# Performance work log

Measured on AMD Instinct MI355X. Metric: run time of the kernel, lower is better.

The kernel has to match this reference:

```python
import jax, jax.numpy as jnp
import numpy as np

B, T, F, H = 4096, 48, 64, 128


def _uniform(key, shape, stdv):
    return jax.random.uniform(key, shape, jnp.float32, -stdv, stdv)


def setup_inputs() -> dict:
    key = jax.random.key(0)
    ks = jax.random.split(key, 24)
    values = jax.random.normal(ks[0], (B, T, F), jnp.float32)
    masks = (jax.random.uniform(ks[1], (B, T, F)) < 0.8).astype(jnp.float32)
    deltas = jax.random.uniform(ks[2], (B, T, F), jnp.float32)
    sH = 1.0 / np.sqrt(H)
    sF = 1.0 / np.sqrt(F)
    inp = {
        "values": values, "masks": masks, "deltas": deltas,
        # TemporalDecay h: W [H, F], b [H] (stdv = 1/sqrt(out=H))
        "Wdh": _uniform(ks[3], (H, F), sH), "bdh": _uniform(ks[4], (H,), sH),
        # TemporalDecay x (diag): W [F, F], b [F]
        "Wdx": _uniform(ks[5], (F, F), sF), "bdx": _uniform(ks[6], (F,), sF),
        # hist_reg: Linear(H -> F)
        "Wh": _uniform(ks[7], (F, H), sH), "bh": _uniform(ks[8], (F,), sH),
        # feat_reg: masked F x F
        "Wf": _uniform(ks[9], (F, F), sF), "bf": _uniform(ks[10], (F,), sF),
        # weight_combine: Linear(2F -> F)
        "Wc": _uniform(ks[11], (F, 2 * F), 1.0 / np.sqrt(2 * F)),
        "bc": _uniform(ks[12], (F,), 1.0 / np.sqrt(2 * F)),
        # LSTMCell(2F -> H): gates in PyTorch order i, f, g, o
        "W_ih": _uniform(ks[13], (4 * H, 2 * F), sH),
        "W_hh": _uniform(ks[14], (4 * H, H), sH),
        "b_ih": _uniform(ks[15], (4 * H,), sH),
        "b_hh": _uniform(ks[16], (4 * H,), sH),
        # out: Linear(H -> 1)
        "Wo": _uniform(ks[17], (1, H), sH), "bo": _uniform(ks[18], (1,), sH),
    }
    return inp


def reference(values, masks, deltas, Wdh, bdh, Wdx, bdx, Wh, bh, Wf, bf,
              Wc, bc, W_ih, W_hh, b_ih, b_hh, Wo, bo):
    impute_weight = 1.0
    b, t, f = values.shape
    h_dim = Wdh.shape[0]
    eye = jnp.eye(f, dtype=values.dtype)
    Wdx_m = Wdx * eye            # diagonal temporal decay
    Wf_m = Wf * (1.0 - eye)

    def step(carry, xt):
        h, c, loss = carry
        x, m, d = xt  # each [B, F]
        gamma_h = jnp.exp(-jax.nn.relu(d @ Wdh.T + bdh))        # [B, H]
        gamma_x = jnp.exp(-jax.nn.relu(d @ Wdx_m.T + bdx))      # [B, F]
        h = h * gamma_h
        x_h = h @ Wh.T + bh
        denom = jnp.sum(m) + 1e-5
        loss = loss + jnp.sum(jnp.abs(x - x_h) * m) / denom
        x_c = m * x + (1.0 - m) * x_h
        z_h = x_c @ Wf_m.T + bf
        loss = loss + jnp.sum(jnp.abs(x - z_h) * m) / denom
        alpha = jnp.concatenate([gamma_x, m], axis=1) @ Wc.T + bc
        c_h = alpha * z_h + (1.0 - alpha) * x_h
        loss = loss + jnp.sum(jnp.abs(x - c_h) * m) / denom
        c_c = m * x + (1.0 - m) * c_h
        inputs = jnp.concatenate([c_c, m], axis=1)  # [B, 2F]
        gates = inputs @ W_ih.T + b_ih + h @ W_hh.T + b_hh
        i_g, f_g, g_g, o_g = jnp.split(gates, 4, axis=1)
        c = jax.nn.sigmoid(f_g) * c + jax.nn.sigmoid(i_g) * jnp.tanh(g_g)
        h = jax.nn.sigmoid(o_g) * jnp.tanh(c)
        return (h, c, loss), c_c

    init = (jnp.zeros((b, h_dim), values.dtype),
            jnp.zeros((b, h_dim), values.dtype),
            jnp.zeros((), values.dtype))
    xs = (jnp.swapaxes(values, 0, 1),
          jnp.swapaxes(masks, 0, 1),
          jnp.swapaxes(deltas, 0, 1))
    (h, c, x_loss), imps = jax.lax.scan(step, init, xs)
    imputations = jnp.swapaxes(imps, 0, 1)  # [B, T, F]
    predictions = h @ Wo.T + bo             # [B, 1]
    return x_loss * impute_weight, imputations, predictions
```

## Files before the change

### kernel.cpp

```cpp
#include <hip/hip_runtime.h>
#include <hip/hip_bf16.h>
#include <math.h>

#define BB 4096
#define TT 48
#define FF 64
#define HH 128
#define ROWS 16
#define NT 512
#define NBLK (BB / ROWS)

typedef __attribute__((ext_vector_type(8))) short short8;
typedef __attribute__((ext_vector_type(4))) float f32x4;

__device__ __forceinline__ float sigm(float x) { return 1.f / (1.f + __expf(-x)); }
__device__ __forceinline__ float tanh_f(float x) { return 2.f / (1.f + __expf(-2.f * x)) - 1.f; }

__global__ __launch_bounds__(256) void prep_kernel(
    const float* __restrict__ W_ih, const float* __restrict__ W_hh,
    const float* __restrict__ Wdh,  const float* __restrict__ Wh,
    const float* __restrict__ Wf,   const float* __restrict__ Wc,
    __hip_bfloat16* __restrict__ frags) {
    const int idx = blockIdx.x * 256 + threadIdx.x;
    float v;
    if (idx < 131072) {
        const int jj = idx & 7;
        const int lane = (idx >> 3) & 63;
        const int ks = (idx >> 9) & 7;
        const int tile = idx >> 12;
        const int n = tile * 16 + (lane & 15);
        const int k = ks * 32 + ((lane >> 4) << 3) + jj;
        v = (k < 128) ? W_ih[n * 128 + k] : W_hh[n * 128 + (k - 128)];
    } else {
        const int u = idx - 131072;
        const int jj = u & 7;
        const int lane = (u >> 3) & 63;
        const int lq = lane & 15, q8 = (lane >> 4) << 3;
        if (u < 8192) {
            const int ks = (u >> 9) & 1, nt = u >> 10;
            const int n = nt * 16 + lq, k = ks * 32 + q8 + jj;
            v = Wdh[n * 64 + k];
        } else if (u < 16384) {
            const int uu = u - 8192;
            const int ks = (uu >> 9) & 3, nt = uu >> 11;
            const int n = nt * 16 + lq, k = ks * 32 + q8 + jj;
            v = Wh[n * 128 + k];
        } else if (u < 20480) {
            const int uu = u - 16384;
            const int ks = (uu >> 9) & 1, nt = uu >> 10;
            const int n = nt * 16 + lq, k = ks * 32 + q8 + jj;
            v = (k == n) ? 0.f : Wf[n * 64 + k];
        } else {
            const int uu = u - 20480;
            const int ks = (uu >> 9) & 3, nt = uu >> 11;
            const int n = nt * 16 + lq, k = ks * 32 + q8 + jj;
            v = Wc[n * 128 + k];
        }
    }
    frags[idx] = __float2bfloat16(v);
}

__global__ __launch_bounds__(NT, 2) void rits_kernel(
    const float* __restrict__ values, const float* __restrict__ masks,
    const float* __restrict__ deltas,
    const float* __restrict__ Wdx, const float* __restrict__ bdx,
    const float* __restrict__ bdh, const float* __restrict__ bh,
    const float* __restrict__ bf,  const float* __restrict__ bc,
    const float* __restrict__ b_ih, const float* __restrict__ b_hh,
    const float* __restrict__ Wo,  const float* __restrict__ bo,
    const __hip_bfloat16* __restrict__ frags,
    float* __restrict__ ws_msum,
    float* __restrict__ ws_numer,
    float* __restrict__ out_imp, float* __restrict__ out_pred)
{
    __shared__ __hip_bfloat16 dbuf[ROWS][72];
    __shared__ __hip_bfloat16 xcbuf[ROWS][72];
    __shared__ __hip_bfloat16 hbuf[ROWS][136];
    __shared__ __hip_bfloat16 gxm[ROWS][136];
    __shared__ __hip_bfloat16 ccm[ROWS][136];
    __shared__ float x_lds[ROWS][65];
    __shared__ float m_lds[ROWS][65];
    __shared__ float redm[8];
    __shared__ float redl[8];

    const int tid = threadIdx.x;
    const int bid = blockIdx.x;
    const int b0 = bid * ROWS;
    const int lane = tid & 63;
    const int wv = tid >> 6;
    const int quad = lane >> 4;
    const int lq = lane & 15;

    for (int i = tid; i < ROWS * 136; i += NT) ((unsigned short*)hbuf)[i] = 0;

    const float wdx_l = Wdx[lane * (FF + 1)];
    const float bdx_l = bdx[lane];

    const int j_ln = wv * 16 + lq;
    const float bdh_j = bdh[j_ln];
    const float bI = b_ih[j_ln]       + b_hh[j_ln];
    const float bF = b_ih[128 + j_ln] + b_hh[128 + j_ln];
    const float bG = b_ih[256 + j_ln] + b_hh[256 + j_ln];
    const float bO = b_ih[384 + j_ln] + b_hh[384 + j_ln];

    const int f46 = (wv & 3) * 16 + lq;
    const float bh_f = bh[f46];
    const float bf_f = bf[f46];
    const float bc_f = bc[f46];

    const short8* f8 = (const short8*)frags;

    float c_reg[4];
    #pragma unroll
    for (int r = 0; r < 4; ++r) c_reg[r] = 0.f;

    __syncthreads();

    for (int t = 0; t < TT; ++t) {
        float msum_th = 0.f;
        #pragma unroll
        for (int q = 0; q < 2; ++q) {
            const int r = wv + 8 * q;
            const int off = ((b0 + r) * TT + t) * FF + lane;
            const float xv = values[off], mv = masks[off], dv = deltas[off];
            x_lds[r][lane] = xv;
            m_lds[r][lane] = mv;
            msum_th += mv;
            dbuf[r][lane] = __float2bfloat16(dv);
            const float gx = __expf(-fmaxf(fmaf(dv, wdx_l, bdx_l), 0.f));
            gxm[r][lane] = __float2bfloat16(gx);
            const __hip_bfloat16 mb = __float2bfloat16(mv);
            gxm[r][64 + lane] = mb;
            ccm[r][64 + lane] = mb;
        }
        #pragma unroll
        for (int off = 32; off; off >>= 1) msum_th += __shfl_down(msum_th, off, 64);
        if (lane == 0) redm[wv] = msum_th;
        __syncthreads();
        if (tid == 0) {
            float s = 0.f;
            #pragma unroll
            for (int w = 0; w < 8; ++w) s += redm[w];
            ws_msum[t * NBLK + bid] = s;
        }

        {
            f32x4 acc = {0.f, 0.f, 0.f, 0.f};
            #pragma unroll
            for (int ks = 0; ks < 2; ++ks) {
                const short8 a = *(const short8*)&dbuf[lq][ks * 32 + quad * 8];
                const short8 b = f8[16384 + ((wv * 2 + ks) << 6) + lane];
                acc = __builtin_amdgcn_mfma_f32_16x16x32_bf16(a, b, acc, 0, 0, 0);
            }
            #pragma unroll
            for (int r = 0; r < 4; ++r) {
                const int row = quad * 4 + r;
                const float gh = __expf(-fmaxf(acc[r] + bdh_j, 0.f));
                const float hd = __bfloat162float(hbuf[row][j_ln]) * gh;
                hbuf[row][j_ln] = __float2bfloat16(hd);
            }
        }
        __syncthreads();

        float xv_r[4], mv_r[4], xh_r[4];
        float stepsum = 0.f;

        if (wv < 4) {
            f32x4 acc = {0.f, 0.f, 0.f, 0.f};
            #pragma unroll
            for (int ks = 0; ks < 4; ++ks) {
                const short8 a = *(const short8*)&hbuf[lq][ks * 32 + quad * 8];
                const short8 b = f8[17408 + ((wv * 4 + ks) << 6) + lane];
                acc = __builtin_amdgcn_mfma_f32_16x16x32_bf16(a, b, acc, 0, 0, 0);
            }
            #pragma unroll
            for (int r = 0; r < 4; ++r) {
                const int row = quad * 4 + r;
                const float xh = acc[r] + bh_f;
                xh_r[r] = xh;
                const float xv = x_lds[row][f46], mv = m_lds[row][f46];
                xv_r[r] = xv; mv_r[r] = mv;
                stepsum += mv * fabsf(xv - xh);
                xcbuf[row][f46] = __float2bfloat16(fmaf(mv, xv, (1.f - mv) * xh));
            }
        }
        __syncthreads();

        if (wv < 4) {
            f32x4 acc5 = {0.f, 0.f, 0.f, 0.f};
            #pragma unroll
            for (int ks = 0; ks < 2; ++ks) {
                const short8 a = *(const short8*)&xcbuf[lq][ks * 32 + quad * 8];
                const short8 b = f8[18432 + ((wv * 2 + ks) << 6) + lane];
                acc5 = __builtin_amdgcn_mfma_f32_16x16x32_bf16(a, b, acc5, 0, 0, 0);
            }
            f32x4 acc6 = {0.f, 0.f, 0.f, 0.f};
            #pragma unroll
            for (int ks = 0; ks < 4; ++ks) {
                const short8 a = *(const short8*)&gxm[lq][ks * 32 + quad * 8];
                const short8 b = f8[18944 + ((wv * 4 + ks) << 6) + lane];
                acc6 = __builtin_amdgcn_mfma_f32_16x16x32_bf16(a, b, acc6, 0, 0, 0);
            }
            #pragma unroll
            for (int r = 0; r < 4; ++r) {
                const int row = quad * 4 + r;
                const float zh = acc5[r] + bf_f;
                stepsum += mv_r[r] * fabsf(xv_r[r] - zh);
                const float alpha = acc6[r] + bc_f;
                const float ch = fmaf(alpha, zh, (1.f - alpha) * xh_r[r]);
                stepsum += mv_r[r] * fabsf(xv_r[r] - ch);
                const float cc = fmaf(mv_r[r], xv_r[r], (1.f - mv_r[r]) * ch);
                ccm[row][f46] = __float2bfloat16(cc);
                out_imp[((b0 + row) * TT + t) * FF + f46] = cc;
            }
        }
        #pragma unroll
        for (int off = 32; off; off >>= 1) stepsum += __shfl_down(stepsum, off, 64);
        if (lane == 0) redl[wv] = stepsum;
        __syncthreads();
        if (tid == 0) {
            float s = 0.f;
            #pragma unroll
            for (int w = 0; w < 8; ++w) s += redl[w];
            ws_numer[t * NBLK + bid] = s;
        }

        {
            f32x4 acc[4];
            #pragma unroll
            for (int g = 0; g < 4; ++g) acc[g] = (f32x4){0.f, 0.f, 0.f, 0.f};
            #pragma unroll
            for (int ks = 0; ks < 8; ++ks) {
                const short8 a = (ks < 4)
                    ? *(const short8*)&ccm[lq][ks * 32 + quad * 8]
                    : *(const short8*)&hbuf[lq][(ks - 4) * 32 + quad * 8];
                #pragma unroll
                for (int g = 0; g < 4; ++g) {
                    const short8 b = f8[(((g * 8 + wv) * 8 + ks) << 6) + lane];
                    acc[g] = __builtin_amdgcn_mfma_f32_16x16x32_bf16(a, b, acc[g], 0, 0, 0);
                }
            }
            float hnew[4];
            #pragma unroll
            for (int r = 0; r < 4; ++r) {
                const float ig = sigm(acc[0][r] + bI);
                const float fg = sigm(acc[1][r] + bF);
                const float gg = tanh_f(acc[2][r] + bG);
                const float og = sigm(acc[3][r] + bO);
                c_reg[r] = fmaf(fg, c_reg[r], ig * gg);
                hnew[r] = og * tanh_f(c_reg[r]);
            }
            __syncthreads();
            #pragma unroll
            for (int r = 0; r < 4; ++r)
                hbuf[quad * 4 + r][j_ln] = __float2bfloat16(hnew[r]);
        }
        __syncthreads();
    }

    {
        const int r = tid >> 5, l = tid & 31;
        float s = 0.f;
        #pragma unroll
        for (int k = l; k < HH; k += 32) s += __bfloat162float(hbuf[r][k]) * Wo[k];
        #pragma unroll
        for (int off = 16; off; off >>= 1) s += __shfl_down(s, off, 32);
        if (l == 0) out_pred[b0 + r] = s + bo[0];
    }
}

__global__ __launch_bounds__(256) void final_kernel(const float* __restrict__ ws_msum,
                                                    const float* __restrict__ ws_numer,
                                                    float* __restrict__ out_loss) {
    const int tid = threadIdx.x;
    const int lane = tid & 63, wv = tid >> 6;
    __shared__ float red[4];
    float acc = 0.f;
    for (int t = wv; t < TT; t += 4) {
        float ms = 0.f, ns = 0.f;
        #pragma unroll
        for (int c = 0; c < NBLK / 64; ++c) {
            ms += ws_msum[t * NBLK + c * 64 + lane];
            ns += ws_numer[t * NBLK + c * 64 + lane];
        }
        #pragma unroll
        for (int off = 32; off; off >>= 1) {
            ms += __shfl_down(ms, off, 64);
            ns += __shfl_down(ns, off, 64);
        }
        if (lane == 0) acc += ns / (ms + 1e-5f);
    }
    if (lane == 0) red[wv] = acc;
    __syncthreads();
    if (tid == 0) out_loss[0] = red[0] + red[1] + red[2] + red[3];
}

extern "C" void kernel_launch(void* const* d_in, const int* in_sizes, int n_in,
                              void* d_out, int out_size, void* d_ws, size_t ws_size,
                              hipStream_t stream) {
    const float* values = (const float*)d_in[0];
    const float* masks  = (const float*)d_in[1];
    const float* deltas = (const float*)d_in[2];
    const float* Wdh  = (const float*)d_in[3];
    const float* bdh  = (const float*)d_in[4];
    const float* Wdx  = (const float*)d_in[5];
    const float* bdx  = (const float*)d_in[6];
    const float* Wh   = (const float*)d_in[7];
    const float* bh   = (const float*)d_in[8];
    const float* Wf   = (const float*)d_in[9];
    const float* bf   = (const float*)d_in[10];
    const float* Wc   = (const float*)d_in[11];
    const float* bc   = (const float*)d_in[12];
    const float* W_ih = (const float*)d_in[13];
    const float* W_hh = (const float*)d_in[14];
    const float* b_ih = (const float*)d_in[15];
    const float* b_hh = (const float*)d_in[16];
    const float* Wo   = (const float*)d_in[17];
    const float* bo   = (const float*)d_in[18];

    __hip_bfloat16* frags = (__hip_bfloat16*)d_ws;
    float* ws_msum  = (float*)((char*)d_ws + 320 * 1024);
    float* ws_numer = ws_msum + TT * NBLK;

    float* out_loss = (float*)d_out;
    float* out_imp  = out_loss + 1;
    float* out_pred = out_imp + (size_t)BB * TT * FF;

    prep_kernel<<<624, 256, 0, stream>>>(W_ih, W_hh, Wdh, Wh, Wf, Wc, frags);
    rits_kernel<<<NBLK, NT, 0, stream>>>(
        values, masks, deltas, Wdx, bdx, bdh, bh, bf, bc,
        b_ih, b_hh, Wo, bo, frags, ws_msum, ws_numer, out_imp, out_pred);
    final_kernel<<<1, 256, 0, stream>>>(ws_msum, ws_numer, out_loss);
}
```

Baseline: 378.5 us.

## Use FP8 LSTM gate matmul, keep h in registers, prefetch inputs, cut barriers

The LSTM gate weights and activations (c_c, mask, h) are quantised to e4m3 FP8 and the gate matmul uses fp8 MFMA, with the weights held in registers. The hidden state stays in fp32 registers across steps. Small weights are cached in LDS, and the next step's inputs are prefetched. The alpha matmul moves to the idle waves, and per-wave partial sums go straight to the workspace, removing several block reductions and barriers. FP8 quantisation of the recurrent state and inputs risks accuracy drift over 48 steps, and holding 32 weight registers per thread raises register pressure.

```diff
diff --git a/kernel.cpp b/kernel.cpp
--- a/kernel.cpp
+++ b/kernel.cpp
@@ -15,49 +15,60 @@
 
 __device__ __forceinline__ float sigm(float x) { return 1.f / (1.f + __expf(-x)); }
 __device__ __forceinline__ float tanh_f(float x) { return 2.f / (1.f + __expf(-2.f * x)) - 1.f; }
+__device__ __forceinline__ unsigned int f32_to_e4m3(float x) {
+    return (unsigned int)(__builtin_amdgcn_cvt_pk_fp8_f32(x, x, 0, false) & 0xff);
+}
 
 __global__ __launch_bounds__(256) void prep_kernel(
     const float* __restrict__ W_ih, const float* __restrict__ W_hh,
     const float* __restrict__ Wdh,  const float* __restrict__ Wh,
     const float* __restrict__ Wf,   const float* __restrict__ Wc,
-    __hip_bfloat16* __restrict__ frags) {
-    const int idx = blockIdx.x * 256 + threadIdx.x;
-    float v;
-    if (idx < 131072) {
-        const int jj = idx & 7;
-        const int lane = (idx >> 3) & 63;
-        const int ks = (idx >> 9) & 7;
-        const int tile = idx >> 12;
+    unsigned long long* __restrict__ wcat8, __hip_bfloat16* __restrict__ fbf) {
+    const int u = blockIdx.x * 256 + threadIdx.x;
+    if (u < 16384) {
+        const int lane = u & 63, ks = (u >> 6) & 7, tile = u >> 9;
         const int n = tile * 16 + (lane & 15);
-        const int k = ks * 32 + ((lane >> 4) << 3) + jj;
-        v = (k < 128) ? W_ih[n * 128 + k] : W_hh[n * 128 + (k - 128)];
+        const int kb = ks * 32 + ((lane >> 4) << 3);
+        const float* src = (kb < 128) ? (W_ih + n * 128 + kb)
+                                      : (W_hh + n * 128 + kb - 128);
+        unsigned int w0 = 0, w1 = 0;
+        #pragma unroll
+        for (int i = 0; i < 4; ++i) w0 |= f32_to_e4m3(src[i]) << (8 * i);
+        #pragma unroll
+        for (int i = 0; i < 4; ++i) w1 |= f32_to_e4m3(src[4 + i]) << (8 * i);
+        wcat8[u] = ((unsigned long long)w1 << 32) | (unsigned long long)w0;
     } else {
-        const int u = idx - 131072;
-        const int jj = u & 7;
-        const int lane = (u >> 3) & 63;
+        const int c = u - 16384;
+        const int lane = c & 63;
         const int lq = lane & 15, q8 = (lane >> 4) << 3;
-        if (u < 8192) {
-            const int ks = (u >> 9) & 1, nt = u >> 10;
-            const int n = nt * 16 + lq, k = ks * 32 + q8 + jj;
-            v = Wdh[n * 64 + k];
-        } else if (u < 16384) {
-            const int uu = u - 8192;
-            const int ks = (uu >> 9) & 3, nt = uu >> 11;
-            const int n = nt * 16 + lq, k = ks * 32 + q8 + jj;
-            v = Wh[n * 128 + k];
-        } else if (u < 20480) {
-            const int uu = u - 16384;
-            const int ks = (uu >> 9) & 1, nt = uu >> 10;
-            const int n = nt * 16 + lq, k = ks * 32 + q8 + jj;
-            v = (k == n) ? 0.f : Wf[n * 64 + k];
+        const float* src; int n, kb; bool fdiag = false;
+        if (c < 1024) {
+            const int ks = (c >> 6) & 1, tile = c >> 7;
+            n = tile * 16 + lq; kb = ks * 32 + q8; src = Wdh + n * 64 + kb;
+        } else if (c < 2048) {
+            const int cc = c - 1024;
+            const int ks = (cc >> 6) & 3, tile = cc >> 8;
+            n = tile * 16 + lq; kb = ks * 32 + q8; src = Wh + n * 128 + kb;
+        } else if (c < 2560) {
+            const int cc = c - 2048;
+            const int ks = (cc >> 6) & 1, tile = cc >> 7;
+            n = tile * 16 + lq; kb = ks * 32 + q8; src = Wf + n * 64 + kb;
+            fdiag = true;
         } else {
-            const int uu = u - 20480;
-            const int ks = (uu >> 9) & 3, nt = uu >> 11;
-            const int n = nt * 16 + lq, k = ks * 32 + q8 + jj;
-            v = Wc[n * 128 + k];
-        }
-    }
-    frags[idx] = __float2bfloat16(v);
+            const int cc = c - 2560;
+            const int ks = (cc >> 6) & 3, tile = cc >> 8;
+            n = tile * 16 + lq; kb = ks * 32 + q8; src = Wc + n * 128 + kb;
+        }
+        short8 out;
+        #pragma unroll
+        for (int i = 0; i < 8; ++i) {
+            float v = src[i];
+            if (fdiag && (kb + i == n)) v = 0.f;
+            __hip_bfloat16 b = __float2bfloat16(v);
+            out[i] = *(short*)&b;
+        }
+        *(short8*)(fbf + (size_t)(c) * 8) = out;
+    }
 }
 
 __global__ __launch_bounds__(NT, 2) void rits_kernel(
@@ -68,20 +79,22 @@
     const float* __restrict__ bf,  const float* __restrict__ bc,
     const float* __restrict__ b_ih, const float* __restrict__ b_hh,
     const float* __restrict__ Wo,  const float* __restrict__ bo,
-    const __hip_bfloat16* __restrict__ frags,
+    const unsigned long long* __restrict__ wcat8,
+    const __hip_bfloat16* __restrict__ fbf,
     float* __restrict__ ws_msum,
     float* __restrict__ ws_numer,
     float* __restrict__ out_imp, float* __restrict__ out_pred)
 {
-    __shared__ __hip_bfloat16 dbuf[ROWS][72];
-    __shared__ __hip_bfloat16 xcbuf[ROWS][72];
-    __shared__ __hip_bfloat16 hbuf[ROWS][136];
-    __shared__ __hip_bfloat16 gxm[ROWS][136];
-    __shared__ __hip_bfloat16 ccm[ROWS][136];
+    __shared__ __align__(16) __hip_bfloat16 dbuf[ROWS][72];
+    __shared__ __align__(16) __hip_bfloat16 xcbuf[ROWS][72];
+    __shared__ __align__(16) __hip_bfloat16 hbuf16[ROWS][136];
+    __shared__ __align__(16) unsigned char  hbuf8[ROWS][136];
+    __shared__ __align__(16) unsigned char  ccm8[ROWS][136];
+    __shared__ __align__(16) __hip_bfloat16 gxm[ROWS][136];
     __shared__ float x_lds[ROWS][65];
     __shared__ float m_lds[ROWS][65];
-    __shared__ float redm[8];
-    __shared__ float redl[8];
+    __shared__ float alpha_buf[ROWS][68];
+    __shared__ __align__(16) __hip_bfloat16 FC_lds[12288];
 
     const int tid = threadIdx.x;
     const int bid = blockIdx.x;
@@ -91,7 +104,9 @@
     const int quad = lane >> 4;
     const int lq = lane & 15;
 
-    for (int i = tid; i < ROWS * 136; i += NT) ((unsigned short*)hbuf)[i] = 0;
+    for (int i = tid; i < 12288 / 8; i += NT) {
+        *(short8*)(FC_lds + i * 8) = *(const short8*)(fbf + 16384 + (size_t)i * 8);
+    }
 
     const float wdx_l = Wdx[lane * (FF + 1)];
     const float bdx_l = bdx[lane];
@@ -108,70 +123,78 @@
     const float bf_f = bf[f46];
     const float bc_f = bc[f46];
 
-    const short8* f8 = (const short8*)frags;
-
-    float c_reg[4];
+    float h_reg[4], c_reg[4];
     #pragma unroll
-    for (int r = 0; r < 4; ++r) c_reg[r] = 0.f;
-
+    for (int r = 0; r < 4; ++r) { h_reg[r] = 0.f; c_reg[r] = 0.f; }
+
+    float xv_pf[2], mv_pf[2], dv_pf[2];
+    #pragma unroll
+    for (int q = 0; q < 2; ++q) {
+        const int off = ((b0 + wv + 8 * q) * TT + 0) * FF + lane;
+        xv_pf[q] = values[off]; mv_pf[q] = masks[off]; dv_pf[q] = deltas[off];
+    }
     __syncthreads();
 
     for (int t = 0; t < TT; ++t) {
+        short8 bDH[2];
+        #pragma unroll
+        for (int ks = 0; ks < 2; ++ks)
+            bDH[ks] = *(const short8*)(fbf + (size_t)((((wv * 2 + ks) << 6) + lane)) * 8);
+        short8 bH[4];
+        if (wv < 4) {
+            #pragma unroll
+            for (int ks = 0; ks < 4; ++ks)
+                bH[ks] = *(const short8*)(fbf + 8192 + (size_t)(((((wv & 3) * 4 + ks) << 6) + lane)) * 8);
+        }
         float msum_th = 0.f;
         #pragma unroll
         for (int q = 0; q < 2; ++q) {
             const int r = wv + 8 * q;
-            const int off = ((b0 + r) * TT + t) * FF + lane;
-            const float xv = values[off], mv = masks[off], dv = deltas[off];
+            const float xv = xv_pf[q], mv = mv_pf[q], dv = dv_pf[q];
             x_lds[r][lane] = xv;
             m_lds[r][lane] = mv;
             msum_th += mv;
             dbuf[r][lane] = __float2bfloat16(dv);
             const float gx = __expf(-fmaxf(fmaf(dv, wdx_l, bdx_l), 0.f));
             gxm[r][lane] = __float2bfloat16(gx);
-            const __hip_bfloat16 mb = __float2bfloat16(mv);
-            gxm[r][64 + lane] = mb;
-            ccm[r][64 + lane] = mb;
+            gxm[r][64 + lane] = __float2bfloat16(mv);
         }
         #pragma unroll
         for (int off = 32; off; off >>= 1) msum_th += __shfl_down(msum_th, off, 64);
-        if (lane == 0) redm[wv] = msum_th;
         __syncthreads();
-        if (tid == 0) {
-            float s = 0.f;
-            #pragma unroll
-            for (int w = 0; w < 8; ++w) s += redm[w];
-            ws_msum[t * NBLK + bid] = s;
-        }
 
         {
             f32x4 acc = {0.f, 0.f, 0.f, 0.f};
             #pragma unroll
             for (int ks = 0; ks < 2; ++ks) {
                 const short8 a = *(const short8*)&dbuf[lq][ks * 32 + quad * 8];
-                const short8 b = f8[16384 + ((wv * 2 + ks) << 6) + lane];
-                acc = __builtin_amdgcn_mfma_f32_16x16x32_bf16(a, b, acc, 0, 0, 0);
+                acc = __builtin_amdgcn_mfma_f32_16x16x32_bf16(a, bDH[ks], acc, 0, 0, 0);
             }
             #pragma unroll
             for (int r = 0; r < 4; ++r) {
                 const int row = quad * 4 + r;
                 const float gh = __expf(-fmaxf(acc[r] + bdh_j, 0.f));
-                const float hd = __bfloat162float(hbuf[row][j_ln]) * gh;
-                hbuf[row][j_ln] = __float2bfloat16(hd);
+                h_reg[r] *= gh;
+                hbuf16[row][j_ln] = __float2bfloat16(h_reg[r]);
+                hbuf8[row][j_ln] = (unsigned char)f32_to_e4m3(h_reg[r]);
             }
         }
         __syncthreads();
 
+        long wB[32];
+        #pragma unroll
+        for (int g = 0; g < 4; ++g)
+            #pragma unroll
+            for (int ks = 0; ks < 8; ++ks)
+                wB[g * 8 + ks] = (long)wcat8[((((g * 8 + wv) * 8 + ks)) << 6) + lane];
+
         float xv_r[4], mv_r[4], xh_r[4];
-        float stepsum = 0.f;
-
         if (wv < 4) {
             f32x4 acc = {0.f, 0.f, 0.f, 0.f};
             #pragma unroll
             for (int ks = 0; ks < 4; ++ks) {
-                const short8 a = *(const short8*)&hbuf[lq][ks * 32 + quad * 8];
-                const short8 b = f8[17408 + ((wv * 4 + ks) << 6) + lane];
-                acc = __builtin_amdgcn_mfma_f32_16x16x32_bf16(a, b, acc, 0, 0, 0);
+                const short8 a = *(const short8*)&hbuf16[lq][ks * 32 + quad * 8];
+                acc = __builtin_amdgcn_mfma_f32_16x16x32_bf16(a, bH[ks], acc, 0, 0, 0);
             }
             #pragma unroll
             for (int r = 0; r < 4; ++r) {
@@ -180,89 +203,101 @@
                 xh_r[r] = xh;
                 const float xv = x_lds[row][f46], mv = m_lds[row][f46];
                 xv_r[r] = xv; mv_r[r] = mv;
-                stepsum += mv * fabsf(xv - xh);
                 xcbuf[row][f46] = __float2bfloat16(fmaf(mv, xv, (1.f - mv) * xh));
             }
+        } else {
+            f32x4 acc = {0.f, 0.f, 0.f, 0.f};
+            const int wv2 = wv - 4;
+            #pragma unroll
+            for (int ks = 0; ks < 4; ++ks) {
+                const short8 a = *(const short8*)&gxm[lq][ks * 32 + quad * 8];
+                const short8 b = *(const short8*)&FC_lds[4096 + (size_t)((((wv2 * 4 + ks) << 6) + lane)) * 8];
+                acc = __builtin_amdgcn_mfma_f32_16x16x32_bf16(a, b, acc, 0, 0, 0);
+            }
+            #pragma unroll
+            for (int r = 0; r < 4; ++r)
+                alpha_buf[quad * 4 + r][f46] = acc[r] + bc_f;
         }
         __syncthreads();
 
+        float stepsum = 0.f;
+        float cc_r[4];
         if (wv < 4) {
-            f32x4 acc5 = {0.f, 0.f, 0.f, 0.f};
+            f32x4 acc = {0.f, 0.f, 0.f, 0.f};
             #pragma unroll
             for (int ks = 0; ks < 2; ++ks) {
                 const short8 a = *(const short8*)&xcbuf[lq][ks * 32 + quad * 8];
-                const short8 b = f8[18432 + ((wv * 2 + ks) << 6) + lane];
-                acc5 = __builtin_amdgcn_mfma_f32_16x16x32_bf16(a, b, acc5, 0, 0, 0);
-            }
-            f32x4 acc6 = {0.f, 0.f, 0.f, 0.f};
-            #pragma unroll
-            for (int ks = 0; ks < 4; ++ks) {
-                const short8 a = *(const short8*)&gxm[lq][ks * 32 + quad * 8];
-                const short8 b = f8[18944 + ((wv * 4 + ks) << 6) + lane];
-                acc6 = __builtin_amdgcn_mfma_f32_16x16x32_bf16(a, b, acc6, 0, 0, 0);
+                const short8 b = *(const short8*)&FC_lds[(size_t)(((((wv & 3) * 2 + ks) << 6) + lane)) * 8];
+                acc = __builtin_amdgcn_mfma_f32_16x16x32_bf16(a, b, acc, 0, 0, 0);
             }
             #pragma unroll
             for (int r = 0; r < 4; ++r) {
                 const int row = quad * 4 + r;
-                const float zh = acc5[r] + bf_f;
+                const float zh = acc[r] + bf_f;
+                stepsum += mv_r[r] * fabsf(xv_r[r] - xh_r[r]);
                 stepsum += mv_r[r] * fabsf(xv_r[r] - zh);
-                const float alpha = acc6[r] + bc_f;
+                const float alpha = alpha_buf[row][f46];
                 const float ch = fmaf(alpha, zh, (1.f - alpha) * xh_r[r]);
                 stepsum += mv_r[r] * fabsf(xv_r[r] - ch);
                 const float cc = fmaf(mv_r[r], xv_r[r], (1.f - mv_r[r]) * ch);
-                ccm[row][f46] = __float2bfloat16(cc);
-                out_imp[((b0 + row) * TT + t) * FF + f46] = cc;
-            }
-        }
-        #pragma unroll
-        for (int off = 32; off; off >>= 1) stepsum += __shfl_down(stepsum, off, 64);
-        if (lane == 0) redl[wv] = stepsum;
+                cc_r[r] = cc;
+                ccm8[row][f46] = (unsigned char)f32_to_e4m3(cc);
+                ccm8[row][64 + f46] = (unsigned char)f32_to_e4m3(mv_r[r]);
+            }
+            #pragma unroll
+            for (int off = 32; off; off >>= 1) stepsum += __shfl_down(stepsum, off, 64);
+        }
         __syncthreads();
-        if (tid == 0) {
-            float s = 0.f;
-            #pragma unroll
-            for (int w = 0; w < 8; ++w) s += redl[w];
-            ws_numer[t * NBLK + bid] = s;
-        }
-
+
+        if (lane == 0) ws_msum[(t * NBLK + bid) * 8 + wv] = msum_th;
+        if (wv < 4) {
+            if (lane == 0) ws_numer[(t * NBLK + bid) * 4 + wv] = stepsum;
+            #pragma unroll
+            for (int r = 0; r < 4; ++r) {
+                const int row = quad * 4 + r;
+                out_imp[((b0 + row) * TT + t) * FF + f46] = cc_r[r];
+            }
+        }
+        const int tn = (t + 1 < TT) ? t + 1 : t;
+        #pragma unroll
+        for (int q = 0; q < 2; ++q) {
+            const int off = ((b0 + wv + 8 * q) * TT + tn) * FF + lane;
+            xv_pf[q] = values[off]; mv_pf[q] = masks[off]; dv_pf[q] = deltas[off];
+        }
         {
-            f32x4 acc[4];
-            #pragma unroll
-            for (int g = 0; g < 4; ++g) acc[g] = (f32x4){0.f, 0.f, 0.f, 0.f};
+            f32x4 acc7[4];
+            #pragma unroll
+            for (int g = 0; g < 4; ++g) acc7[g] = (f32x4){0.f, 0.f, 0.f, 0.f};
             #pragma unroll
             for (int ks = 0; ks < 8; ++ks) {
-                const short8 a = (ks < 4)
-                    ? *(const short8*)&ccm[lq][ks * 32 + quad * 8]
-                    : *(const short8*)&hbuf[lq][(ks - 4) * 32 + quad * 8];
+                const long a = (ks < 4)
+                    ? *(const long*)&ccm8[lq][ks * 32 + quad * 8]
+                    : *(const long*)&hbuf8[lq][(ks - 4) * 32 + quad * 8];
                 #pragma unroll
-                for (int g = 0; g < 4; ++g) {
-                    const short8 b = f8[(((g * 8 + wv) * 8 + ks) << 6) + lane];
-                    acc[g] = __builtin_amdgcn_mfma_f32_16x16x32_bf16(a, b, acc[g], 0, 0, 0);
-                }
-            }
-            float hnew[4];
-            #pragma unroll
-            for (int r = 0; r < 4; ++r) {
-                const float ig = sigm(acc[0][r] + bI);
-                const float fg = sigm(acc[1][r] + bF);
-                const float gg = tanh_f(acc[2][r] + bG);
-                const float og = sigm(acc[3][r] + bO);
+                for (int g = 0; g < 4; ++g)
+                    acc7[g] = __builtin_amdgcn_mfma_f32_16x16x32_fp8_fp8(a, wB[g * 8 + ks], acc7[g], 0, 0, 0);
+            }
+            #pragma unroll
+            for (int r = 0; r < 4; ++r) {
+                const float ig = sigm(acc7[0][r] + bI);
+                const float fg = sigm(acc7[1][r] + bF);
+                const float gg = tanh_f(acc7[2][r] + bG);
+                const float og = sigm(acc7[3][r] + bO);
                 c_reg[r] = fmaf(fg, c_reg[r], ig * gg);
-                hnew[r] = og * tanh_f(c_reg[r]);
-            }
-            __syncthreads();
-            #pragma unroll
-            for (int r = 0; r < 4; ++r)
-                hbuf[quad * 4 + r][j_ln] = __float2bfloat16(hnew[r]);
-        }
-        __syncthreads();
-    }
-
+                h_reg[r] = og * tanh_f(c_reg[r]);
+            }
+        }
+    }
+
+    #pragma unroll
+    for (int r = 0; r < 4; ++r)
+        hbuf16[quad * 4 + r][j_ln] = __float2bfloat16(h_reg[r]);
+    __syncthreads();
     {
         const int r = tid >> 5, l = tid & 31;
         float s = 0.f;
         #pragma unroll
-        for (int k = l; k < HH; k += 32) s += __bfloat162float(hbuf[r][k]) * Wo[k];
+        for (int k = l; k < HH; k += 32) s += __bfloat162float(hbuf16[r][k]) * Wo[k];
         #pragma unroll
         for (int off = 16; off; off >>= 1) s += __shfl_down(s, off, 32);
         if (l == 0) out_pred[b0 + r] = s + bo[0];
@@ -273,16 +308,13 @@
                                                     const float* __restrict__ ws_numer,
                                                     float* __restrict__ out_loss) {
     const int tid = threadIdx.x;
-    const int lane = tid & 63, wv = tid >> 6;
+    const int lane = tid & 63, wvf = tid >> 6;
     __shared__ float red[4];
     float acc = 0.f;
-    for (int t = wv; t < TT; t += 4) {
+    for (int t = wvf; t < TT; t += 4) {
         float ms = 0.f, ns = 0.f;
-        #pragma unroll
-        for (int c = 0; c < NBLK / 64; ++c) {
-            ms += ws_msum[t * NBLK + c * 64 + lane];
-            ns += ws_numer[t * NBLK + c * 64 + lane];
-        }
+        for (int i = lane; i < NBLK * 8; i += 64) ms += ws_msum[t * NBLK * 8 + i];
+        for (int i = lane; i < NBLK * 4; i += 64) ns += ws_numer[t * NBLK * 4 + i];
         #pragma unroll
         for (int off = 32; off; off >>= 1) {
             ms += __shfl_down(ms, off, 64);
@@ -290,7 +322,7 @@
         }
         if (lane == 0) acc += ns / (ms + 1e-5f);
     }
-    if (lane == 0) red[wv] = acc;
+    if (lane == 0) red[wvf] = acc;
     __syncthreads();
     if (tid == 0) out_loss[0] = red[0] + red[1] + red[2] + red[3];
 }
@@ -318,17 +350,18 @@
     const float* Wo   = (const float*)d_in[17];
     const float* bo   = (const float*)d_in[18];
 
-    __hip_bfloat16* frags = (__hip_bfloat16*)d_ws;
-    float* ws_msum  = (float*)((char*)d_ws + 320 * 1024);
-    float* ws_numer = ws_msum + TT * NBLK;
+    unsigned long long* wcat8 = (unsigned long long*)d_ws;
+    __hip_bfloat16* fbf = (__hip_bfloat16*)((char*)d_ws + 131072);
+    float* ws_msum  = (float*)((char*)d_ws + 188416);
+    float* ws_numer = (float*)((char*)d_ws + 581632);
 
     float* out_loss = (float*)d_out;
     float* out_imp  = out_loss + 1;
     float* out_pred = out_imp + (size_t)BB * TT * FF;
 
-    prep_kernel<<<624, 256, 0, stream>>>(W_ih, W_hh, Wdh, Wh, Wf, Wc, frags);
+    prep_kernel<<<78, 256, 0, stream>>>(W_ih, W_hh, Wdh, Wh, Wf, Wc, wcat8, fbf);
     rits_kernel<<<NBLK, NT, 0, stream>>>(
         values, masks, deltas, Wdx, bdx, bdh, bh, bf, bc,
-        b_ih, b_hh, Wo, bo, frags, ws_msum, ws_numer, out_imp, out_pred);
+        b_ih, b_hh, Wo, bo, wcat8, fbf, ws_msum, ws_numer, out_imp, out_pred);
     final_kernel<<<1, 256, 0, stream>>>(ws_msum, ws_numer, out_loss);
 }
```

Result: slower. 479.5 us (+26.7%).
